# Optimization experiments

Hardware: AMD Instinct MI355X
Metric: run time of the kernel (lower is better)

## Reference

```python
import jax, jax.numpy as jnp
import numpy as np

N = 100000   # nodes per type
D = 128      # embedding_dim
H = 4        # attn_heads
C = D // H   # out_channels
E = 400000   # edges per relation
NEG_SLOPE = 0.01  # F.leaky_relu default


def setup_inputs() -> dict:
    key = jax.random.key(0)
    ks = jax.random.split(key, 24)
    inp = {
        "featA": jax.random.normal(ks[0], (N, D), jnp.float32),
        "featB": jax.random.normal(ks[1], (N, D), jnp.float32),
        "src_aa": jax.random.randint(ks[2], (E,), 0, N, jnp.int32),
        "dst_aa": jax.random.randint(ks[3], (E,), 0, N, jnp.int32),
        "src_ab": jax.random.randint(ks[4], (E,), 0, N, jnp.int32),
        "dst_ab": jax.random.randint(ks[5], (E,), 0, N, jnp.int32),
        "src_ba": jax.random.randint(ks[6], (E,), 0, N, jnp.int32),
        "dst_ba": jax.random.randint(ks[7], (E,), 0, N, jnp.int32),
    }
    # per-layer params: W stacked over node types [A=0, B=1]; attn over metapaths [aa=0, ab=1, ba=2]
    i = 8
    for t in range(2):
        inp[f"Wl{t}"] = jax.random.normal(ks[i + 0], (2, D, D), jnp.float32) * 0.05
        inp[f"bl{t}"] = jnp.zeros((2, D), jnp.float32)
        inp[f"Wr{t}"] = jax.random.normal(ks[i + 1], (2, D, D), jnp.float32) * 0.05
        inp[f"br{t}"] = jnp.zeros((2, D), jnp.float32)
        inp[f"al{t}"] = jax.random.normal(ks[i + 2], (3, H, C), jnp.float32) * 0.1
        inp[f"ar{t}"] = jax.random.normal(ks[i + 3], (3, H, C), jnp.float32) * 0.1
        i += 4
    return inp


def _segment_softmax(att, dst, n):
    # att: [E, H]; softmax over incoming edges per destination node, per head
    m = jax.ops.segment_max(att, dst, num_segments=n)
    e = jnp.exp(att - m[dst])
    s = jax.ops.segment_sum(e, dst, num_segments=n)
    return e / s[dst]


def _relation(k_src, v_dst, src, dst, a_l, a_r, n_dst):
    # per-edge attention: leaky_relu((k_src*attn_l).sum + (v_dst*attn_r).sum)
    att = jax.nn.leaky_relu((k_src[src] * a_l).sum(-1) + (v_dst[dst] * a_r).sum(-1), NEG_SLOPE)  # [E,H]
    alpha = _segment_softmax(att, dst, n_dst)                                                    # [E,H]
    # message h = v of the DESTINATION node (as in edge_attention), weighted-summed per dst
    h = jax.ops.segment_sum(alpha[..., None] * v_dst[dst], dst, num_segments=n_dst)              # [Nd,H,C]
    return h.reshape(n_dst, -1)


def _layer(hA, hB, Wl, bl, Wr, br, al, ar, edges):
    src_aa, dst_aa, src_ab, dst_ab, src_ba, dst_ba = edges
    kA = (hA @ Wl[0] + bl[0]).reshape(N, H, C)
    kB = (hB @ Wl[1] + bl[1]).reshape(N, H, C)
    vA = (hA @ Wr[0] + br[0]).reshape(N, H, C)
    vB = (hB @ Wr[1] + br[1]).reshape(N, H, C)
    h_aa = _relation(kA, vA, src_aa, dst_aa, al[0], ar[0], N)  # A -> A
    h_ab = _relation(kA, vB, src_ab, dst_ab, al[1], ar[1], N)  # A -> B
    h_ba = _relation(kB, vA, src_ba, dst_ba, al[2], ar[2], N)  # B -> A
    # mean over stacked relation outputs + the node's own v, then relu
    outA = jax.nn.relu((h_aa + h_ba + vA.reshape(N, D)) / 3.0)
    outB = jax.nn.relu((h_ab + vB.reshape(N, D)) / 2.0)
    return outA, outB


def reference(featA, featB, src_aa, dst_aa, src_ab, dst_ab, src_ba, dst_ba,
              Wl0, bl0, Wr0, br0, al0, ar0, Wl1, bl1, Wr1, br1, al1, ar1):
    edges = (src_aa, dst_aa, src_ab, dst_ab, src_ba, dst_ba)
    hA, hB = _layer(featA, featB, Wl0, bl0, Wr0, br0, al0, ar0, edges)
    hA, hB = _layer(hA, hB, Wl1, bl1, Wr1, br1, al1, ar1, edges)
    return jnp.stack([hA, hB])  # [2, N, D]
```

## Files before the change

### kernel.cpp

```cpp
#include <hip/hip_runtime.h>
#include <hip/hip_bf16.h>

#define NN 100000
#define EE 400000
#define STRIPS 6250
#define WAVES_TOT 1024

typedef unsigned short u16;
typedef __attribute__((ext_vector_type(4))) float floatx4;
typedef __attribute__((ext_vector_type(8))) short shortx8;
typedef __attribute__((ext_vector_type(4))) unsigned short ushortx4;
typedef __attribute__((ext_vector_type(8))) unsigned short ushortx8;

__device__ __forceinline__ u16 f2bf(float f) {
    unsigned u = __float_as_uint(f);
    u += 0x7FFFu + ((u >> 16) & 1u);
    return (u16)(u >> 16);
}

__global__ __launch_bounds__(256) void mark(
    const int4* __restrict__ daa, const int4* __restrict__ dab,
    const int4* __restrict__ dba, unsigned char* __restrict__ m) {
    int i = blockIdx.x * 256 + threadIdx.x;
    if (i < EE / 4) {
        int4 a = daa[i], b = dab[i], c = dba[i];
        m[a.x] = 1; m[a.y] = 1; m[a.z] = 1; m[a.w] = 1;
        m[NN + b.x] = 1; m[NN + b.y] = 1; m[NN + b.z] = 1; m[NN + b.w] = 1;
        m[2 * NN + c.x] = 1; m[2 * NN + c.y] = 1; m[2 * NN + c.z] = 1; m[2 * NN + c.w] = 1;
    }
}

__global__ __launch_bounds__(256, 2) void fused2(
    const float* __restrict__ featA, const float* __restrict__ featB,
    const float* __restrict__ Wr0, const float* __restrict__ Wr1,
    const float* __restrict__ br0, const float* __restrict__ br1,
    const unsigned char* __restrict__ masks, float* __restrict__ out) {
    __shared__ u16 lds[40960];

    const int type = blockIdx.x >> 8;
    const int bid = blockIdx.x & 255;
    const float* feat = type ? featB : featA;
    const float* W0 = Wr0 + type * 16384;
    const float* W1 = Wr1 + type * 16384;
    const float* b0 = br0 + type * 128;
    const float* b1 = br1 + type * 128;
    float* outp = out + (size_t)type * NN * 128;

    const int t = threadIdx.x;
    const int wave = t >> 6, lane = t & 63;
    const int quad = lane >> 4, mrow = lane & 15;
    const int gw = bid * 4 + wave;

    int s = gw;
    floatx4 pf[8];
    unsigned char pm0 = 0, pm1 = 0;
    {
        const float* arow = feat + (size_t)(s * 16 + mrow) * 128;
#pragma unroll
        for (int ks = 0; ks < 4; ++ks) {
            pf[2 * ks]     = *(const floatx4*)(arow + ks * 32 + quad * 8);
            pf[2 * ks + 1] = *(const floatx4*)(arow + ks * 32 + quad * 8 + 4);
        }
        int row = s * 16 + mrow;
        if (type) pm0 = masks[NN + row];
        else { pm0 = masks[row]; pm1 = masks[2 * NN + row]; }
    }

#pragma unroll
    for (int i = 0; i < 16; ++i) {
        int g = i * 256 + t;
        int mat = g >> 11;
        int gg = g & 2047;
        int chunk = gg >> 6;
        int l2 = gg & 63;
        int kbase = (chunk >> 3) * 32 + (l2 >> 4) * 8;
        int n = (chunk & 7) * 16 + (l2 & 15);
        const float* W = mat ? W1 : W0;
        ushortx8 p;
#pragma unroll
        for (int j = 0; j < 8; ++j) p[j] = f2bf(W[(kbase + j) * 128 + n]);
        *(ushortx8*)&lds[mat * 16384 + chunk * 512 + l2 * 8] = p;
    }
    __syncthreads();

    const int h1base = 32768 + wave * 2048;

    for (;;) {
        shortx8 bfrag[4];
#pragma unroll
        for (int ks = 0; ks < 4; ++ks) {
            floatx4 f0 = pf[2 * ks], f1 = pf[2 * ks + 1];
            union { shortx8 v; u16 u[8]; } uu;
            uu.u[0] = f2bf(f0[0]); uu.u[1] = f2bf(f0[1]);
            uu.u[2] = f2bf(f0[2]); uu.u[3] = f2bf(f0[3]);
            uu.u[4] = f2bf(f1[0]); uu.u[5] = f2bf(f1[1]);
            uu.u[6] = f2bf(f1[2]); uu.u[7] = f2bf(f1[3]);
            bfrag[ks] = uu.v;
        }
        const float scl = type ? (1.0f + (float)pm0) * 0.5f
                               : (1.0f + (float)pm0 + (float)pm1) * (1.0f / 3.0f);
        const float s2 = scl * scl;
        const int row = s * 16 + mrow;

        const int sn = s + WAVES_TOT;
        const bool more = sn < STRIPS;
        if (more) {
            const float* arow = feat + (size_t)(sn * 16 + mrow) * 128;
#pragma unroll
            for (int ks = 0; ks < 4; ++ks) {
                pf[2 * ks]     = *(const floatx4*)(arow + ks * 32 + quad * 8);
                pf[2 * ks + 1] = *(const floatx4*)(arow + ks * 32 + quad * 8 + 4);
            }
            int nrow = sn * 16 + mrow;
            if (type) pm0 = masks[NN + nrow];
            else { pm0 = masks[nrow]; pm1 = masks[2 * NN + nrow]; }
        }

        floatx4 acc[8];
#pragma unroll
        for (int nt = 0; nt < 8; ++nt) acc[nt] = (floatx4){0.f, 0.f, 0.f, 0.f};
#pragma unroll
        for (int ks = 0; ks < 4; ++ks)
#pragma unroll
            for (int nt = 0; nt < 8; ++nt) {
                shortx8 af = *(const shortx8*)&lds[((ks * 8 + nt) << 9) + lane * 8];
                acc[nt] = __builtin_amdgcn_mfma_f32_16x16x32_bf16(af, bfrag[ks], acc[nt], 0, 0, 0);
            }

#pragma unroll
        for (int nt = 0; nt < 8; ++nt) {
            floatx4 bv = *(const floatx4*)(b0 + nt * 16 + quad * 4);
            ushortx4 p;
#pragma unroll
            for (int r = 0; r < 4; ++r)
                p[r] = f2bf(fmaxf(acc[nt][r] + bv[r], 0.0f));
            int q2 = (2 * nt + (quad >> 1)) & 3;
            *(ushortx4*)&lds[h1base + (nt >> 1) * 512 + q2 * 128 + mrow * 8 + (quad & 1) * 4] = p;
        }

        shortx8 h1b[4];
#pragma unroll
        for (int ks = 0; ks < 4; ++ks)
            h1b[ks] = *(const shortx8*)&lds[h1base + ks * 512 + lane * 8];

        floatx4 acc2[8];
#pragma unroll
        for (int nt = 0; nt < 8; ++nt) acc2[nt] = (floatx4){0.f, 0.f, 0.f, 0.f};
#pragma unroll
        for (int ks = 0; ks < 4; ++ks)
#pragma unroll
            for (int nt = 0; nt < 8; ++nt) {
                shortx8 af = *(const shortx8*)&lds[16384 + ((ks * 8 + nt) << 9) + lane * 8];
                acc2[nt] = __builtin_amdgcn_mfma_f32_16x16x32_bf16(af, h1b[ks], acc2[nt], 0, 0, 0);
            }

        float* orow = outp + (size_t)row * 128;
#pragma unroll
        for (int nt = 0; nt < 8; ++nt) {
            floatx4 bv = *(const floatx4*)(b1 + nt * 16 + quad * 4);
            floatx4 o;
#pragma unroll
            for (int r = 0; r < 4; ++r)
                o[r] = fmaxf(s2 * acc2[nt][r] + scl * bv[r], 0.0f);
            *(floatx4*)(orow + nt * 16 + quad * 4) = o;
        }

        if (!more) break;
        s = sn;
    }
}

extern "C" void kernel_launch(void* const* d_in, const int* in_sizes, int n_in,
                              void* d_out, int out_size, void* d_ws, size_t ws_size,
                              hipStream_t stream) {
    (void)in_sizes; (void)n_in; (void)out_size; (void)ws_size;
    const float* featA = (const float*)d_in[0];
    const float* featB = (const float*)d_in[1];
    const int* dst_aa = (const int*)d_in[3];
    const int* dst_ab = (const int*)d_in[5];
    const int* dst_ba = (const int*)d_in[7];
    const float* Wr0 = (const float*)d_in[10];
    const float* br0 = (const float*)d_in[11];
    const float* Wr1 = (const float*)d_in[16];
    const float* br1 = (const float*)d_in[17];

    unsigned char* masks = (unsigned char*)d_ws;

    hipMemsetAsync(masks, 0, (size_t)3 * NN, stream);
    mark<<<(EE / 4 + 255) / 256, 256, 0, stream>>>(
        (const int4*)dst_aa, (const int4*)dst_ab, (const int4*)dst_ba, masks);
    fused2<<<512, 256, 0, stream>>>(featA, featB, Wr0, Wr1, br0, br1,
                                    masks, (float*)d_out);
}
```

Before: 238.0 us.

## Precompute bf16 weights once in mark kernel, use 1024-thread blocks, nontemporal stores

Weight fp32-to-bf16 conversion and swizzling move out of each fused block into extra blocks of the mark kernel, which write a packed bf16 copy to workspace. The fused kernel then only copies that copy into LDS. Blocks grow from 256 to 1024 threads with 128 KB of LDS, so 256 blocks share the same weights across 16 waves each. Output stores become nontemporal. This cuts the redundant strided weight reads and conversion per block, at the cost of a larger workspace and heavier LDS use per block.

```diff
diff --git a/kernel.cpp b/kernel.cpp
--- a/kernel.cpp
+++ b/kernel.cpp
@@ -1,10 +1,10 @@
 #include <hip/hip_runtime.h>
-#include <hip/hip_bf16.h>
 
 #define NN 100000
 #define EE 400000
 #define STRIPS 6250
-#define WAVES_TOT 1024
+#define WAVES_TOT 2048
+#define MARK_BLOCKS 391
 
 typedef unsigned short u16;
 typedef __attribute__((ext_vector_type(4))) float floatx4;
@@ -18,30 +18,46 @@
     return (u16)(u >> 16);
 }
 
-__global__ __launch_bounds__(256) void mark(
+__global__ __launch_bounds__(256) void mark_conv(
     const int4* __restrict__ daa, const int4* __restrict__ dab,
-    const int4* __restrict__ dba, unsigned char* __restrict__ m) {
-    int i = blockIdx.x * 256 + threadIdx.x;
-    if (i < EE / 4) {
-        int4 a = daa[i], b = dab[i], c = dba[i];
-        m[a.x] = 1; m[a.y] = 1; m[a.z] = 1; m[a.w] = 1;
-        m[NN + b.x] = 1; m[NN + b.y] = 1; m[NN + b.z] = 1; m[NN + b.w] = 1;
-        m[2 * NN + c.x] = 1; m[2 * NN + c.y] = 1; m[2 * NN + c.z] = 1; m[2 * NN + c.w] = 1;
-    }
-}
-
-__global__ __launch_bounds__(256, 2) void fused2(
+    const int4* __restrict__ dba,
+    const float* __restrict__ Wr0, const float* __restrict__ Wr1,
+    unsigned char* __restrict__ m, u16* __restrict__ wbf) {
+    const int blk = blockIdx.x;
+    if (blk < MARK_BLOCKS) {
+        int i = blk * 256 + threadIdx.x;
+        if (i < EE / 4) {
+            int4 a = daa[i], bb = dab[i], c = dba[i];
+            m[a.x] = 1; m[a.y] = 1; m[a.z] = 1; m[a.w] = 1;
+            m[NN + bb.x] = 1; m[NN + bb.y] = 1; m[NN + bb.z] = 1; m[NN + bb.w] = 1;
+            m[2 * NN + c.x] = 1; m[2 * NN + c.y] = 1; m[2 * NN + c.z] = 1; m[2 * NN + c.w] = 1;
+        }
+    } else {
+        int flat = (blk - MARK_BLOCKS) * 256 + threadIdx.x;
+        int type = flat >> 12;
+        int mat = (flat >> 11) & 1;
+        int chunk = (flat >> 6) & 31;
+        int l2 = flat & 63;
+        int kbase = (chunk >> 3) * 32 + (l2 >> 4) * 8;
+        int n = (chunk & 7) * 16 + (l2 & 15);
+        const float* W = (mat ? Wr1 : Wr0) + type * 16384;
+        ushortx8 p;
+#pragma unroll
+        for (int j = 0; j < 8; ++j) p[j] = f2bf(W[(kbase + j) * 128 + n]);
+        *(ushortx8*)&wbf[((type * 2 + mat) << 14) + chunk * 512 + l2 * 8] = p;
+    }
+}
+
+__global__ __launch_bounds__(1024, 4) void fused2(
     const float* __restrict__ featA, const float* __restrict__ featB,
-    const float* __restrict__ Wr0, const float* __restrict__ Wr1,
+    const u16* __restrict__ wbf,
     const float* __restrict__ br0, const float* __restrict__ br1,
     const unsigned char* __restrict__ masks, float* __restrict__ out) {
-    __shared__ u16 lds[40960];
-
-    const int type = blockIdx.x >> 8;
-    const int bid = blockIdx.x & 255;
+    __shared__ u16 lds[65536];
+
+    const int type = blockIdx.x >> 7;
+    const int bid = blockIdx.x & 127;
     const float* feat = type ? featB : featA;
-    const float* W0 = Wr0 + type * 16384;
-    const float* W1 = Wr1 + type * 16384;
     const float* b0 = br0 + type * 128;
     const float* b1 = br1 + type * 128;
     float* outp = out + (size_t)type * NN * 128;
@@ -49,7 +65,7 @@
     const int t = threadIdx.x;
     const int wave = t >> 6, lane = t & 63;
     const int quad = lane >> 4, mrow = lane & 15;
-    const int gw = bid * 4 + wave;
+    const int gw = bid * 16 + wave;
 
     int s = gw;
     floatx4 pf[8];
@@ -66,20 +82,13 @@
         else { pm0 = masks[row]; pm1 = masks[2 * NN + row]; }
     }
 
-#pragma unroll
-    for (int i = 0; i < 16; ++i) {
-        int g = i * 256 + t;
-        int mat = g >> 11;
-        int gg = g & 2047;
-        int chunk = gg >> 6;
-        int l2 = gg & 63;
-        int kbase = (chunk >> 3) * 32 + (l2 >> 4) * 8;
-        int n = (chunk & 7) * 16 + (l2 & 15);
-        const float* W = mat ? W1 : W0;
-        ushortx8 p;
-#pragma unroll
-        for (int j = 0; j < 8; ++j) p[j] = f2bf(W[(kbase + j) * 128 + n]);
-        *(ushortx8*)&lds[mat * 16384 + chunk * 512 + l2 * 8] = p;
+    {
+        const ushortx8* __restrict__ wsrc = (const ushortx8*)(wbf + ((size_t)type << 15));
+#pragma unroll
+        for (int i = 0; i < 4; ++i) {
+            int idx = i * 1024 + t;
+            *(ushortx8*)&lds[idx * 8] = wsrc[idx];
+        }
     }
     __syncthreads();
 
@@ -162,7 +171,7 @@
 #pragma unroll
             for (int r = 0; r < 4; ++r)
                 o[r] = fmaxf(s2 * acc2[nt][r] + scl * bv[r], 0.0f);
-            *(floatx4*)(orow + nt * 16 + quad * 4) = o;
+            __builtin_nontemporal_store(o, (floatx4*)(orow + nt * 16 + quad * 4));
         }
 
         if (!more) break;
@@ -185,10 +194,12 @@
     const float* br1 = (const float*)d_in[17];
 
     unsigned char* masks = (unsigned char*)d_ws;
+    u16* wbf = (u16*)((char*)d_ws + (size_t)3 * NN);
 
     hipMemsetAsync(masks, 0, (size_t)3 * NN, stream);
-    mark<<<(EE / 4 + 255) / 256, 256, 0, stream>>>(
-        (const int4*)dst_aa, (const int4*)dst_ab, (const int4*)dst_ba, masks);
-    fused2<<<512, 256, 0, stream>>>(featA, featB, Wr0, Wr1, br0, br1,
-                                    masks, (float*)d_out);
-}
+    mark_conv<<<MARK_BLOCKS + 32, 256, 0, stream>>>(
+        (const int4*)dst_aa, (const int4*)dst_ab, (const int4*)dst_ba,
+        Wr0, Wr1, masks, wbf);
+    fused2<<<256, 1024, 0, stream>>>(featA, featB, wbf, br0, br1,
+                                     masks, (float*)d_out);
+}
```

Result: slower. 310.4 us (+30.4%).
